# Kernel optimization log

Hardware: AMD Instinct MI355X
Metric: run time of the kernel (lower is better)

## Reference

```python
import jax, jax.numpy as jnp
import numpy as np

D = 768      # hidden size (hardcoded in module)
H = 8        # MHA heads
DH = D // H  # head dim = 96
SLOPE = 0.01 # LeakyReLU default negative slope
NEG = -1e9


def _leaky(x):
    return jnp.where(x >= 0, x, SLOPE * x)


def setup_inputs() -> dict:
    key = jax.random.key(0)
    ks = jax.random.split(key, 20)
    B, S, T, C, L = 32, 2048, 64, 512, 16
    seq = jax.random.normal(ks[0], (B, S, D), dtype=jnp.float32)
    tab_ids = jax.random.randint(ks[1], (B, T, L), 0, S, dtype=jnp.int32)
    col_ids = jax.random.randint(ks[2], (B, C, L), 0, S, dtype=jnp.int32)
    # contiguous column->table assignment (8 cols/table), mirrors cumulative
    # slicing by column_number_in_each_table and keeps every table non-empty
    t_of_c = jnp.broadcast_to(jnp.repeat(jnp.arange(T, dtype=jnp.int32), C // T), (B, C))
    g = lambda k, sh: (jax.random.normal(k, sh, dtype=jnp.float32) * 0.02)
    return {
        "sequence_embeddings": seq,
        "table_token_ids": tab_ids,
        "column_token_ids": col_ids,
        "table_of_column": t_of_c,
        "W_tab_pool": g(ks[3], (D, D)), "b_tab_pool": g(ks[4], (D,)),
        "W_col_pool": g(ks[5], (D, D)), "b_col_pool": g(ks[6], (D,)),
        "in_proj_w": g(ks[7], (3 * D, D)), "in_proj_b": g(ks[8], (3 * D,)),
        "out_proj_w": g(ks[9], (D, D)), "out_proj_b": g(ks[10], (D,)),
        "W_t1": g(ks[11], (D, 256)), "b_t1": g(ks[12], (256,)),
        "W_t2": g(ks[13], (256, 2)), "b_t2": g(ks[14], (2,)),
        "W_c1": g(ks[15], (D, 256)), "b_c1": g(ks[16], (256,)),
        "W_c2": g(ks[17], (256, 2)), "b_c2": g(ks[18], (2,)),
    }


def reference(sequence_embeddings, table_token_ids, column_token_ids, table_of_column,
              W_tab_pool, b_tab_pool, W_col_pool, b_col_pool,
              in_proj_w, in_proj_b, out_proj_w, out_proj_b,
              W_t1, b_t1, W_t2, b_t2, W_c1, b_c1, W_c2, b_c2):
    B, T = table_token_ids.shape[:2]
    C = column_token_ids.shape[1]
    bi = jnp.arange(B)[:, None, None]
    # ragged span sum-pooling (gather + segment sum)
    tab = sequence_embeddings[bi, table_token_ids].sum(axis=2)   # [B,T,D]
    col = sequence_embeddings[bi, column_token_ids].sum(axis=2)  # [B,C,D]
    tab = _leaky(tab @ W_tab_pool + b_tab_pool)
    col = _leaky(col @ W_col_pool + b_col_pool)
    # per-table cross-attention (table query over its own columns), batched + masked
    Wq, Wk, Wv = jnp.split(in_proj_w, 3, axis=0)
    bq, bk, bv = jnp.split(in_proj_b, 3, axis=0)
    q = (tab @ Wq.T + bq).reshape(B, T, H, DH)
    k = (col @ Wk.T + bk).reshape(B, C, H, DH)
    v = (col @ Wv.T + bv).reshape(B, C, H, DH)
    scores = jnp.einsum('bthd,bchd->bhtc', q, k) / jnp.sqrt(jnp.float32(DH))
    mask = table_of_column[:, None, None, :] == jnp.arange(T, dtype=table_of_column.dtype)[None, None, :, None]
    attn = jax.nn.softmax(jnp.where(mask, scores, NEG), axis=-1)
    ctx = jnp.einsum('bhtc,bchd->bthd', attn, v).reshape(B, T, D)
    tab = tab + (ctx @ out_proj_w.T + out_proj_b)
    tab = tab / jnp.maximum(jnp.linalg.norm(tab, axis=-1, keepdims=True), 1e-12)
    # classification heads (dropout in eval mode = identity)
    t_logits = _leaky(tab @ W_t1 + b_t1) @ W_t2 + b_t2  # [B,T,2]
    c_logits = _leaky(col @ W_c1 + b_c1) @ W_c2 + b_c2  # [B,C,2]
    return jnp.concatenate([t_logits, c_logits], axis=1)  # [B,T+C,2]
```

## Files before the change

### kernel.cpp

```cpp
#include <hip/hip_runtime.h>
#include <hip/hip_bf16.h>

constexpr int Bc = 32;
constexpr int Sc = 2048;
constexpr int Tc = 64;
constexpr int Cc = 512;
constexpr int Lc = 16;
constexpr int Dc = 768;
constexpr int Hc = 8;
constexpr int DHc = 96;

typedef __attribute__((ext_vector_type(4))) float f32x4;
typedef __attribute__((ext_vector_type(8))) short bf16x8;

__device__ inline unsigned short f2bf(float f) {
  __hip_bfloat16 h = __float2bfloat16(f);
  return *reinterpret_cast<unsigned short*>(&h);
}
__device__ inline float bf2f(__hip_bfloat16 h) { return __bfloat162float(h); }

#define GLDS16(gp, lp)                                                        \
  __builtin_amdgcn_global_load_lds(                                           \
      (const __attribute__((address_space(1))) void*)(gp),                    \
      (__attribute__((address_space(3))) void*)(lp), 16, 0, 0)

__global__ __launch_bounds__(256) void pool_kernel(
    const float* __restrict__ seq, const int* __restrict__ tab_ids,
    const int* __restrict__ col_ids, __hip_bfloat16* __restrict__ tabp,
    __hip_bfloat16* __restrict__ colp) {
  int w = threadIdx.x >> 6, l = threadIdx.x & 63;
  int row = blockIdx.x * 4 + w;
  int b = row / (Tc + Cc), r = row % (Tc + Cc);
  const int* ids;
  __hip_bfloat16* outp;
  if (r < Tc) {
    ids = tab_ids + ((size_t)b * Tc + r) * Lc;
    outp = tabp + ((size_t)b * Tc + r) * Dc;
  } else {
    int c = r - Tc;
    ids = col_ids + ((size_t)b * Cc + c) * Lc;
    outp = colp + ((size_t)b * Cc + c) * Dc;
  }
  float4 a0 = {0, 0, 0, 0}, a1 = {0, 0, 0, 0}, a2 = {0, 0, 0, 0};
#pragma unroll
  for (int t = 0; t < Lc; ++t) {
    const float4* p =
        reinterpret_cast<const float4*>(seq + ((size_t)b * Sc + ids[t]) * Dc);
    float4 v0 = p[l], v1 = p[l + 64], v2 = p[l + 128];
    a0.x += v0.x; a0.y += v0.y; a0.z += v0.z; a0.w += v0.w;
    a1.x += v1.x; a1.y += v1.y; a1.z += v1.z; a1.w += v1.w;
    a2.x += v2.x; a2.y += v2.y; a2.z += v2.z; a2.w += v2.w;
  }
  ushort4* ob = reinterpret_cast<ushort4*>(outp);
  ob[l] = make_ushort4(f2bf(a0.x), f2bf(a0.y), f2bf(a0.z), f2bf(a0.w));
  ob[l + 64] = make_ushort4(f2bf(a1.x), f2bf(a1.y), f2bf(a1.z), f2bf(a1.w));
  ob[l + 128] = make_ushort4(f2bf(a2.x), f2bf(a2.y), f2bf(a2.z), f2bf(a2.w));
}

__global__ __launch_bounds__(256) void convt_kernel(
    const float* __restrict__ in, __hip_bfloat16* __restrict__ out, int K,
    int N) {
  __shared__ float t[32][33];
  int bx = blockIdx.x * 32, by = blockIdx.y * 32;
  int x = threadIdx.x & 31, y = threadIdx.x >> 5;
#pragma unroll
  for (int i = 0; i < 32; i += 8) t[y + i][x] = in[(size_t)(by + y + i) * N + bx + x];
  __syncthreads();
#pragma unroll
  for (int i = 0; i < 32; i += 8)
    out[(size_t)(bx + y + i) * K + by + x] = __float2bfloat16(t[x][y + i]);
}

__global__ __launch_bounds__(256) void conv_kernel(
    const float4* __restrict__ in, ushort4* __restrict__ out, int n4) {
  int i = blockIdx.x * 256 + threadIdx.x;
  if (i < n4) {
    float4 v = in[i];
    out[i] = make_ushort4(f2bf(v.x), f2bf(v.y), f2bf(v.z), f2bf(v.w));
  }
}

template <int OUTMODE, bool LEAKY>
__global__ __launch_bounds__(256) void gemm_bf16(
    const __hip_bfloat16* __restrict__ A, const __hip_bfloat16* __restrict__ Bt,
    const float* __restrict__ bias, __hip_bfloat16* __restrict__ Obf,
    float* __restrict__ Of32, int M, int N, int K) {
  constexpr int BM = 128, BN = 128, BK = 32;
  __shared__ __hip_bfloat16 As[BM * BK];
  __shared__ __hip_bfloat16 Bs[BN * BK];
  int tid = threadIdx.x;
  int row0 = blockIdx.y * BM, col0 = blockIdx.x * BN;
  int w = tid >> 6, l = tid & 63;
  int wr = (w >> 1) * 64, wc = (w & 1) * 64;
  f32x4 acc[4][4];
#pragma unroll
  for (int m = 0; m < 4; ++m)
#pragma unroll
    for (int n = 0; n < 4; ++n) acc[m][n] = f32x4{0.f, 0.f, 0.f, 0.f};

  int srow = tid >> 2;
  int skk = (tid & 3) * 8;
  const __hip_bfloat16* gA = A + (size_t)(row0 + srow) * K + skk;
  const __hip_bfloat16* gB = Bt + (size_t)(col0 + srow) * K + skk;
  char* lA = (char*)As + tid * 16;
  char* lB = (char*)Bs + tid * 16;
  int lr = l & 15, lk = (l >> 4) * 8;

  for (int k0 = 0; k0 < K; k0 += BK) {
    GLDS16(gA + k0, lA);
    GLDS16(gA + k0 + (size_t)64 * K, lA + 4096);
    GLDS16(gB + k0, lB);
    GLDS16(gB + k0 + (size_t)64 * K, lB + 4096);
    __syncthreads();
    bf16x8 af[4], bfr[4];
#pragma unroll
    for (int m = 0; m < 4; ++m)
      af[m] = *reinterpret_cast<const bf16x8*>(&As[(wr + m * 16 + lr) * BK + lk]);
#pragma unroll
    for (int n = 0; n < 4; ++n)
      bfr[n] = *reinterpret_cast<const bf16x8*>(&Bs[(wc + n * 16 + lr) * BK + lk]);
#pragma unroll
    for (int m = 0; m < 4; ++m)
#pragma unroll
      for (int n = 0; n < 4; ++n)
        acc[m][n] = __builtin_amdgcn_mfma_f32_16x16x32_bf16(af[m], bfr[n],
                                                            acc[m][n], 0, 0, 0);
    __syncthreads();
  }

  int colI = l & 15, rowb = (l >> 4) * 4;
#pragma unroll
  for (int m = 0; m < 4; ++m) {
#pragma unroll
    for (int n = 0; n < 4; ++n) {
      int c = col0 + wc + n * 16 + colI;
      float bv = bias ? bias[c] : 0.f;
#pragma unroll
      for (int j = 0; j < 4; ++j) {
        int r = row0 + wr + m * 16 + rowb + j;
        float v = acc[m][n][j] + bv;
        if (LEAKY) v = v >= 0.f ? v : 0.01f * v;
        if (OUTMODE == 0 || OUTMODE == 2)
          Obf[(size_t)r * N + c] = __float2bfloat16(v);
        if (OUTMODE == 1 || OUTMODE == 2) Of32[(size_t)r * N + c] = v;
      }
    }
  }
}

__global__ __launch_bounds__(256) void bucket_kernel(
    const int* __restrict__ t_of_c, int* __restrict__ col_sorted,
    int* __restrict__ offs) {
  int b = blockIdx.x, tid = threadIdx.x;
  __shared__ int cnt[Tc];
  __shared__ int cur[Tc + 1];
  if (tid < Tc) cnt[tid] = 0;
  __syncthreads();
  for (int c = tid; c < Cc; c += 256) atomicAdd(&cnt[t_of_c[b * Cc + c]], 1);
  __syncthreads();
  if (tid == 0) {
    int off = 0;
    for (int t = 0; t < Tc; ++t) {
      cur[t] = off;
      off += cnt[t];
    }
    cur[Tc] = off;
  }
  __syncthreads();
  if (tid <= Tc) offs[b * (Tc + 1) + tid] = cur[tid];
  __syncthreads();
  for (int c = tid; c < Cc; c += 256) {
    int t = t_of_c[b * Cc + c];
    int pos = atomicAdd(&cur[t], 1);
    col_sorted[b * Cc + pos] = c;
  }
}

__global__ __launch_bounds__(256) void attn_kernel(
    const __hip_bfloat16* __restrict__ q, const __hip_bfloat16* __restrict__ kv,
    const int* __restrict__ col_sorted, const int* __restrict__ offs,
    __hip_bfloat16* __restrict__ ctx) {
  int b = blockIdx.x / Tc;
  int t = blockIdx.x % Tc;
  __shared__ float qs[Dc];
  __shared__ float pbuf[Hc][Cc];
  __shared__ float den[Hc];
  __shared__ int cols_s[Cc];
  int tid = threadIdx.x;
  for (int i = tid; i < Dc; i += 256)
    qs[i] = bf2f(q[((size_t)b * Tc + t) * Dc + i]);
  int o0 = offs[b * (Tc + 1) + t];
  int o1 = offs[b * (Tc + 1) + t + 1];
  int n = o1 - o0;
  for (int i = tid; i < n; i += 256)
    cols_s[i] = col_sorted[(size_t)b * Cc + o0 + i];
  __syncthreads();
  int h = tid >> 5, l32 = tid & 31;
  const float scale = 0.10206207261596577f;
  if (n > 0) {
    float lmax = -3.0e38f;
    for (int j = l32; j < n; j += 32) {
      const __hip_bfloat16* kr = kv + ((size_t)b * Cc + cols_s[j]) * 1536 + h * DHc;
      float s = 0.f;
#pragma unroll 8
      for (int d = 0; d < DHc; ++d) s += qs[h * DHc + d] * bf2f(kr[d]);
      s *= scale;
      pbuf[h][j] = s;
      lmax = fmaxf(lmax, s);
    }
#pragma unroll
    for (int m = 16; m >= 1; m >>= 1) lmax = fmaxf(lmax, __shfl_xor(lmax, m));
    float lsum = 0.f;
    for (int j = l32; j < n; j += 32) {
      float e = __expf(pbuf[h][j] - lmax);
      pbuf[h][j] = e;
      lsum += e;
    }
#pragma unroll
    for (int m = 16; m >= 1; m >>= 1) lsum += __shfl_xor(lsum, m);
    if (l32 == 0) den[h] = lsum;
  }
  __syncthreads();
#pragma unroll
  for (int rep = 0; rep < 3; ++rep) {
    int d = l32 + rep * 32;
    float acc = 0.f;
    if (n > 0) {
      for (int j = 0; j < n; ++j)
        acc += pbuf[h][j] *
               bf2f(kv[((size_t)b * Cc + cols_s[j]) * 1536 + 768 + h * DHc + d]);
      acc /= den[h];
    } else {
      for (int c = 0; c < Cc; ++c)
        acc += bf2f(kv[((size_t)b * Cc + c) * 1536 + 768 + h * DHc + d]);
      acc *= (1.0f / Cc);
    }
    ctx[((size_t)b * Tc + t) * Dc + h * DHc + d] = __float2bfloat16(acc);
  }
}

__global__ __launch_bounds__(256) void addnorm_kernel(
    const float* __restrict__ tab, const float* __restrict__ proj,
    __hip_bfloat16* __restrict__ tabn) {
  int row = blockIdx.x;
  int tid = threadIdx.x;
  size_t base = (size_t)row * Dc;
  float x0 = tab[base + tid] + proj[base + tid];
  float x1 = tab[base + tid + 256] + proj[base + tid + 256];
  float x2 = tab[base + tid + 512] + proj[base + tid + 512];
  float ss = x0 * x0 + x1 * x1 + x2 * x2;
#pragma unroll
  for (int m = 32; m >= 1; m >>= 1) ss += __shfl_xor(ss, m);
  __shared__ float red[4];
  int wave = tid >> 6, lane = tid & 63;
  if (lane == 0) red[wave] = ss;
  __syncthreads();
  float total = red[0] + red[1] + red[2] + red[3];
  float sc = 1.0f / fmaxf(sqrtf(total), 1e-12f);
  tabn[base + tid] = __float2bfloat16(x0 * sc);
  tabn[base + tid + 256] = __float2bfloat16(x1 * sc);
  tabn[base + tid + 512] = __float2bfloat16(x2 * sc);
}

__global__ __launch_bounds__(256) void head2_kernel(
    const float* __restrict__ h1t, const float* __restrict__ h1c,
    const float* __restrict__ W_t2, const float* __restrict__ b_t2,
    const float* __restrict__ W_c2, const float* __restrict__ b_c2,
    float* __restrict__ out) {
  int w = threadIdx.x >> 6;
  int lane = threadIdx.x & 63;
  int row = blockIdx.x * 4 + w;
  int b = row / (Tc + Cc);
  int r = row % (Tc + Cc);
  const float* h1;
  const float* W2;
  const float* b2;
  if (r < Tc) {
    h1 = h1t + ((size_t)b * Tc + r) * 256;
    W2 = W_t2;
    b2 = b_t2;
  } else {
    h1 = h1c + ((size_t)b * Cc + (r - Tc)) * 256;
    W2 = W_c2;
    b2 = b_c2;
  }
  float a0 = 0.f, a1 = 0.f;
  for (int i = lane; i < 256; i += 64) {
    float x = h1[i];
    a0 += x * W2[2 * i];
    a1 += x * W2[2 * i + 1];
  }
#pragma unroll
  for (int m = 32; m >= 1; m >>= 1) {
    a0 += __shfl_xor(a0, m);
    a1 += __shfl_xor(a1, m);
  }
  if (lane == 0) {
    out[(size_t)row * 2] = a0 + b2[0];
    out[(size_t)row * 2 + 1] = a1 + b2[1];
  }
}

extern "C" void kernel_launch(void* const* d_in, const int* in_sizes, int n_in,
                              void* d_out, int out_size, void* d_ws,
                              size_t ws_size, hipStream_t stream) {
  const float* seq = (const float*)d_in[0];
  const int* tab_ids = (const int*)d_in[1];
  const int* col_ids = (const int*)d_in[2];
  const int* t_of_c = (const int*)d_in[3];
  const float* W_tab_pool = (const float*)d_in[4];
  const float* b_tab_pool = (const float*)d_in[5];
  const float* W_col_pool = (const float*)d_in[6];
  const float* b_col_pool = (const float*)d_in[7];
  const float* in_proj_w = (const float*)d_in[8];
  const float* in_proj_b = (const float*)d_in[9];
  const float* out_proj_w = (const float*)d_in[10];
  const float* out_proj_b = (const float*)d_in[11];
  const float* W_t1 = (const float*)d_in[12];
  const float* b_t1 = (const float*)d_in[13];
  const float* W_t2 = (const float*)d_in[14];
  const float* b_t2 = (const float*)d_in[15];
  const float* W_c1 = (const float*)d_in[16];
  const float* b_c1 = (const float*)d_in[17];
  const float* W_c2 = (const float*)d_in[18];
  const float* b_c2 = (const float*)d_in[19];
  float* out = (float*)d_out;

  typedef __hip_bfloat16 bf;
  char* p = (char*)d_ws;
  auto alloc = [&](size_t bytes) -> char* {
    char* r = p;
    p += (bytes + 255) & ~(size_t)255;
    return r;
  };
  const size_t nBT = (size_t)Bc * Tc;
  const size_t nBC = (size_t)Bc * Cc;
  bf* tabp = (bf*)alloc(nBT * Dc * 2);
  bf* colp = (bf*)alloc(nBC * Dc * 2);
  bf* tabb_bf = (bf*)alloc(nBT * Dc * 2);
  float* tabb_f = (float*)alloc(nBT * Dc * 4);
  bf* colb = (bf*)alloc(nBC * Dc * 2);
  bf* qb = (bf*)alloc(nBT * Dc * 2);
  bf* kvb = (bf*)alloc(nBC * 1536 * 2);
  bf* ctxb = (bf*)alloc(nBT * Dc * 2);
  float* projb = (float*)alloc(nBT * Dc * 4);
  bf* tabn = (bf*)alloc(nBT * Dc * 2);
  float* h1t = (float*)alloc(nBT * 256 * 4);
  float* h1c = (float*)alloc(nBC * 256 * 4);
  bf* wtab_t = (bf*)alloc((size_t)Dc * Dc * 2);
  bf* wcol_t = (bf*)alloc((size_t)Dc * Dc * 2);
  bf* winproj = (bf*)alloc((size_t)3 * Dc * Dc * 2);
  bf* woutproj = (bf*)alloc((size_t)Dc * Dc * 2);
  bf* wt1_t = (bf*)alloc((size_t)256 * Dc * 2);
  bf* wc1_t = (bf*)alloc((size_t)256 * Dc * 2);
  int* col_sorted = (int*)alloc(nBC * 4);
  int* offs = (int*)alloc((size_t)Bc * (Tc + 1) * 4);

  convt_kernel<<<dim3(Dc / 32, Dc / 32), 256, 0, stream>>>(W_tab_pool, wtab_t, Dc, Dc);
  convt_kernel<<<dim3(Dc / 32, Dc / 32), 256, 0, stream>>>(W_col_pool, wcol_t, Dc, Dc);
  conv_kernel<<<(3 * Dc * Dc / 4) / 256, 256, 0, stream>>>(
      (const float4*)in_proj_w, (ushort4*)winproj, 3 * Dc * Dc / 4);
  conv_kernel<<<(Dc * Dc / 4) / 256, 256, 0, stream>>>(
      (const float4*)out_proj_w, (ushort4*)woutproj, Dc * Dc / 4);
  convt_kernel<<<dim3(256 / 32, Dc / 32), 256, 0, stream>>>(W_t1, wt1_t, Dc, 256);
  convt_kernel<<<dim3(256 / 32, Dc / 32), 256, 0, stream>>>(W_c1, wc1_t, Dc, 256);

  bucket_kernel<<<Bc, 256, 0, stream>>>(t_of_c, col_sorted, offs);
  pool_kernel<<<Bc * (Tc + Cc) / 4, 256, 0, stream>>>(seq, tab_ids, col_ids,
                                                      tabp, colp);
  gemm_bf16<2, true><<<dim3(Dc / 128, nBT / 128), 256, 0, stream>>>(
      tabp, wtab_t, b_tab_pool, tabb_bf, tabb_f, nBT, Dc, Dc);
  gemm_bf16<0, true><<<dim3(Dc / 128, nBC / 128), 256, 0, stream>>>(
      colp, wcol_t, b_col_pool, colb, nullptr, nBC, Dc, Dc);
  gemm_bf16<0, false><<<dim3(Dc / 128, nBT / 128), 256, 0, stream>>>(
      tabb_bf, winproj, in_proj_b, qb, nullptr, nBT, Dc, Dc);
  gemm_bf16<0, false><<<dim3(1536 / 128, nBC / 128), 256, 0, stream>>>(
      colb, winproj + (size_t)Dc * Dc, in_proj_b + Dc, kvb, nullptr, nBC, 1536,
      Dc);
  attn_kernel<<<Bc * Tc, 256, 0, stream>>>(qb, kvb, col_sorted, offs, ctxb);
  gemm_bf16<1, false><<<dim3(Dc / 128, nBT / 128), 256, 0, stream>>>(
      ctxb, woutproj, out_proj_b, nullptr, projb, nBT, Dc, Dc);
  addnorm_kernel<<<nBT, 256, 0, stream>>>(tabb_f, projb, tabn);
  gemm_bf16<1, true><<<dim3(256 / 128, nBT / 128), 256, 0, stream>>>(
      tabn, wt1_t, b_t1, nullptr, h1t, nBT, 256, Dc);
  gemm_bf16<1, true><<<dim3(256 / 128, nBC / 128), 256, 0, stream>>>(
      colb, wc1_t, b_c1, nullptr, h1c, nBC, 256, Dc);
  head2_kernel<<<(Bc * (Tc + Cc)) / 4, 256, 0, stream>>>(h1t, h1c, W_t2, b_t2,
                                                         W_c2, b_c2, out);
}
```

Measured before the change: 627.4 us.

## Fuse weight prep, fold head2 into GEMM epilogue, rework attention and GEMM BK

Merges the six weight-conversion launches and the output bias initialisation into one prep kernel. Fuses the second classifier layer into the first head GEMM's epilogue, which reduces across lanes and atomically adds into the output, so the h1 buffers and the head2 kernel go away. Rewrites attention so 8-lane groups use vectorised bf16 loads with q held in registers for both QK and PV, and doubles the GEMM K-tile to 64. It also swizzles the pool kernel's block order. Atomics make the output summation order nondeterministic, and the larger tile raises LDS use.

```diff
diff --git a/kernel.cpp b/kernel.cpp
--- a/kernel.cpp
+++ b/kernel.cpp
@@ -12,27 +12,82 @@
 
 typedef __attribute__((ext_vector_type(4))) float f32x4;
 typedef __attribute__((ext_vector_type(8))) short bf16x8;
+typedef __hip_bfloat16 bf;
 
 __device__ inline unsigned short f2bf(float f) {
   __hip_bfloat16 h = __float2bfloat16(f);
   return *reinterpret_cast<unsigned short*>(&h);
 }
-__device__ inline float bf2f(__hip_bfloat16 h) { return __bfloat162float(h); }
+__device__ inline float us2f(unsigned short u) {
+  return __uint_as_float(((unsigned)u) << 16);
+}
 
 #define GLDS16(gp, lp)                                                        \
   __builtin_amdgcn_global_load_lds(                                           \
       (const __attribute__((address_space(1))) void*)(gp),                    \
       (__attribute__((address_space(3))) void*)(lp), 16, 0, 0)
 
+__device__ inline void transpose32(const float* __restrict__ in,
+                                   bf* __restrict__ outp, int K, int N,
+                                   int ti, float (*t)[33]) {
+  int nx = N >> 5;
+  int bx = (ti % nx) * 32, by = (ti / nx) * 32;
+  int x = threadIdx.x & 31, y = threadIdx.x >> 5;
+#pragma unroll
+  for (int i = 0; i < 32; i += 8)
+    t[y + i][x] = in[(size_t)(by + y + i) * N + bx + x];
+  __syncthreads();
+#pragma unroll
+  for (int i = 0; i < 32; i += 8)
+    outp[(size_t)(bx + y + i) * K + by + x] = __float2bfloat16(t[x][y + i]);
+}
+
+__global__ __launch_bounds__(256) void prep_kernel(
+    const float* __restrict__ W_tab_pool, const float* __restrict__ W_col_pool,
+    const float* __restrict__ W_t1, const float* __restrict__ W_c1,
+    const float* __restrict__ in_proj_w, const float* __restrict__ out_proj_w,
+    const float* __restrict__ b_t2, const float* __restrict__ b_c2,
+    bf* __restrict__ wtab_t, bf* __restrict__ wcol_t, bf* __restrict__ wt1_t,
+    bf* __restrict__ wc1_t, bf* __restrict__ winproj, bf* __restrict__ woutproj,
+    float* __restrict__ outd) {
+  __shared__ float t[32][33];
+  int blk = blockIdx.x, tid = threadIdx.x;
+  if (blk < 576) {
+    transpose32(W_tab_pool, wtab_t, Dc, Dc, blk, t);
+  } else if (blk < 1152) {
+    transpose32(W_col_pool, wcol_t, Dc, Dc, blk - 576, t);
+  } else if (blk < 1344) {
+    transpose32(W_t1, wt1_t, Dc, 256, blk - 1152, t);
+  } else if (blk < 1536) {
+    transpose32(W_c1, wc1_t, Dc, 256, blk - 1344, t);
+  } else if (blk < 3264) {
+    int i = (blk - 1536) * 256 + tid;
+    float4 v = reinterpret_cast<const float4*>(in_proj_w)[i];
+    reinterpret_cast<ushort4*>(winproj)[i] =
+        make_ushort4(f2bf(v.x), f2bf(v.y), f2bf(v.z), f2bf(v.w));
+  } else if (blk < 3840) {
+    int i = (blk - 3264) * 256 + tid;
+    float4 v = reinterpret_cast<const float4*>(out_proj_w)[i];
+    reinterpret_cast<ushort4*>(woutproj)[i] =
+        make_ushort4(f2bf(v.x), f2bf(v.y), f2bf(v.z), f2bf(v.w));
+  } else {
+    int e = (blk - 3840) * 256 + tid;
+    int i = e & 1;
+    int r = (e >> 1) % (Tc + Cc);
+    outd[e] = (r < Tc) ? b_t2[i] : b_c2[i];
+  }
+}
+
 __global__ __launch_bounds__(256) void pool_kernel(
     const float* __restrict__ seq, const int* __restrict__ tab_ids,
-    const int* __restrict__ col_ids, __hip_bfloat16* __restrict__ tabp,
-    __hip_bfloat16* __restrict__ colp) {
+    const int* __restrict__ col_ids, bf* __restrict__ tabp,
+    bf* __restrict__ colp) {
+  int swz = (blockIdx.x & 7) * 576 + (blockIdx.x >> 3);
   int w = threadIdx.x >> 6, l = threadIdx.x & 63;
-  int row = blockIdx.x * 4 + w;
+  int row = swz * 4 + w;
   int b = row / (Tc + Cc), r = row % (Tc + Cc);
   const int* ids;
-  __hip_bfloat16* outp;
+  bf* outp;
   if (r < Tc) {
     ids = tab_ids + ((size_t)b * Tc + r) * Lc;
     outp = tabp + ((size_t)b * Tc + r) * Dc;
@@ -43,9 +98,9 @@
   }
   float4 a0 = {0, 0, 0, 0}, a1 = {0, 0, 0, 0}, a2 = {0, 0, 0, 0};
 #pragma unroll
-  for (int t = 0; t < Lc; ++t) {
+  for (int tix = 0; tix < Lc; ++tix) {
     const float4* p =
-        reinterpret_cast<const float4*>(seq + ((size_t)b * Sc + ids[t]) * Dc);
+        reinterpret_cast<const float4*>(seq + ((size_t)b * Sc + ids[tix]) * Dc);
     float4 v0 = p[l], v1 = p[l + 64], v2 = p[l + 128];
     a0.x += v0.x; a0.y += v0.y; a0.z += v0.z; a0.w += v0.w;
     a1.x += v1.x; a1.y += v1.y; a1.z += v1.z; a1.w += v1.w;
@@ -57,37 +112,15 @@
   ob[l + 128] = make_ushort4(f2bf(a2.x), f2bf(a2.y), f2bf(a2.z), f2bf(a2.w));
 }
 
-__global__ __launch_bounds__(256) void convt_kernel(
-    const float* __restrict__ in, __hip_bfloat16* __restrict__ out, int K,
-    int N) {
-  __shared__ float t[32][33];
-  int bx = blockIdx.x * 32, by = blockIdx.y * 32;
-  int x = threadIdx.x & 31, y = threadIdx.x >> 5;
-#pragma unroll
-  for (int i = 0; i < 32; i += 8) t[y + i][x] = in[(size_t)(by + y + i) * N + bx + x];
-  __syncthreads();
-#pragma unroll
-  for (int i = 0; i < 32; i += 8)
-    out[(size_t)(bx + y + i) * K + by + x] = __float2bfloat16(t[x][y + i]);
-}
-
-__global__ __launch_bounds__(256) void conv_kernel(
-    const float4* __restrict__ in, ushort4* __restrict__ out, int n4) {
-  int i = blockIdx.x * 256 + threadIdx.x;
-  if (i < n4) {
-    float4 v = in[i];
-    out[i] = make_ushort4(f2bf(v.x), f2bf(v.y), f2bf(v.z), f2bf(v.w));
-  }
-}
-
-template <int OUTMODE, bool LEAKY>
+template <int OUTMODE, bool LEAKY, int LOG2RPB>
 __global__ __launch_bounds__(256) void gemm_bf16(
-    const __hip_bfloat16* __restrict__ A, const __hip_bfloat16* __restrict__ Bt,
-    const float* __restrict__ bias, __hip_bfloat16* __restrict__ Obf,
-    float* __restrict__ Of32, int M, int N, int K) {
-  constexpr int BM = 128, BN = 128, BK = 32;
-  __shared__ __hip_bfloat16 As[BM * BK];
-  __shared__ __hip_bfloat16 Bs[BN * BK];
+    const bf* __restrict__ A, const bf* __restrict__ Bt,
+    const float* __restrict__ bias, bf* __restrict__ Obf,
+    float* __restrict__ Of32, const float* __restrict__ w2,
+    float* __restrict__ outd, int out_base, int M, int N, int K) {
+  constexpr int BM = 128, BN = 128, BK = 64;
+  __shared__ bf As[BM * BK];
+  __shared__ bf Bs[BN * BK];
   int tid = threadIdx.x;
   int row0 = blockIdx.y * BM, col0 = blockIdx.x * BN;
   int w = tid >> 6, l = tid & 63;
@@ -98,37 +131,94 @@
 #pragma unroll
     for (int n = 0; n < 4; ++n) acc[m][n] = f32x4{0.f, 0.f, 0.f, 0.f};
 
-  int srow = tid >> 2;
-  int skk = (tid & 3) * 8;
-  const __hip_bfloat16* gA = A + (size_t)(row0 + srow) * K + skk;
-  const __hip_bfloat16* gB = Bt + (size_t)(col0 + srow) * K + skk;
+  int srow = tid >> 3, skk = (tid & 7) * 8;
+  const bf* gA = A + (size_t)(row0 + srow) * K + skk;
+  const bf* gB = Bt + (size_t)(col0 + srow) * K + skk;
   char* lA = (char*)As + tid * 16;
   char* lB = (char*)Bs + tid * 16;
   int lr = l & 15, lk = (l >> 4) * 8;
 
   for (int k0 = 0; k0 < K; k0 += BK) {
-    GLDS16(gA + k0, lA);
-    GLDS16(gA + k0 + (size_t)64 * K, lA + 4096);
-    GLDS16(gB + k0, lB);
-    GLDS16(gB + k0 + (size_t)64 * K, lB + 4096);
+#pragma unroll
+    for (int c = 0; c < 4; ++c) {
+      GLDS16(gA + k0 + (size_t)c * 32 * K, lA + c * 4096);
+      GLDS16(gB + k0 + (size_t)c * 32 * K, lB + c * 4096);
+    }
     __syncthreads();
-    bf16x8 af[4], bfr[4];
+    bf16x8 af[2][4], bfr[2][4];
+#pragma unroll
+    for (int ks = 0; ks < 2; ++ks) {
+#pragma unroll
+      for (int m = 0; m < 4; ++m)
+        af[ks][m] = *reinterpret_cast<const bf16x8*>(
+            &As[(wr + m * 16 + lr) * BK + ks * 32 + lk]);
+#pragma unroll
+      for (int n = 0; n < 4; ++n)
+        bfr[ks][n] = *reinterpret_cast<const bf16x8*>(
+            &Bs[(wc + n * 16 + lr) * BK + ks * 32 + lk]);
+    }
+#pragma unroll
+    for (int ks = 0; ks < 2; ++ks)
+#pragma unroll
+      for (int m = 0; m < 4; ++m)
+#pragma unroll
+        for (int n = 0; n < 4; ++n)
+          acc[m][n] = __builtin_amdgcn_mfma_f32_16x16x32_bf16(
+              af[ks][m], bfr[ks][n], acc[m][n], 0, 0, 0);
+    __syncthreads();
+  }
+
+  int colI = l & 15, rowb = (l >> 4) * 4;
+  if (OUTMODE == 3) {
+    float w20[4], w21[4], bv[4];
+#pragma unroll
+    for (int n = 0; n < 4; ++n) {
+      int c = col0 + wc + n * 16 + colI;
+      w20[n] = w2[c * 2];
+      w21[n] = w2[c * 2 + 1];
+      bv[n] = bias[c];
+    }
+    float p0[4][4], p1[4][4];
 #pragma unroll
     for (int m = 0; m < 4; ++m)
-      af[m] = *reinterpret_cast<const bf16x8*>(&As[(wr + m * 16 + lr) * BK + lk]);
-#pragma unroll
-    for (int n = 0; n < 4; ++n)
-      bfr[n] = *reinterpret_cast<const bf16x8*>(&Bs[(wc + n * 16 + lr) * BK + lk]);
+#pragma unroll
+      for (int j = 0; j < 4; ++j) { p0[m][j] = 0.f; p1[m][j] = 0.f; }
 #pragma unroll
     for (int m = 0; m < 4; ++m)
 #pragma unroll
       for (int n = 0; n < 4; ++n)
-        acc[m][n] = __builtin_amdgcn_mfma_f32_16x16x32_bf16(af[m], bfr[n],
-                                                            acc[m][n], 0, 0, 0);
-    __syncthreads();
-  }
-
-  int colI = l & 15, rowb = (l >> 4) * 4;
+#pragma unroll
+        for (int j = 0; j < 4; ++j) {
+          float v = acc[m][n][j] + bv[n];
+          v = v >= 0.f ? v : 0.01f * v;
+          p0[m][j] += v * w20[n];
+          p1[m][j] += v * w21[n];
+        }
+#pragma unroll
+    for (int m = 0; m < 4; ++m)
+#pragma unroll
+      for (int j = 0; j < 4; ++j) {
+#pragma unroll
+        for (int msk = 1; msk <= 8; msk <<= 1) {
+          p0[m][j] += __shfl_xor(p0[m][j], msk);
+          p1[m][j] += __shfl_xor(p1[m][j], msk);
+        }
+      }
+    if (colI == 0) {
+#pragma unroll
+      for (int m = 0; m < 4; ++m)
+#pragma unroll
+        for (int j = 0; j < 4; ++j) {
+          int grow = row0 + wr + m * 16 + rowb + j;
+          int bb = grow >> LOG2RPB;
+          int rr = grow & ((1 << LOG2RPB) - 1);
+          int orow = bb * (Tc + Cc) + out_base + rr;
+          atomicAdd(&outd[(size_t)orow * 2], p0[m][j]);
+          atomicAdd(&outd[(size_t)orow * 2 + 1], p1[m][j]);
+        }
+    }
+    return;
+  }
 #pragma unroll
   for (int m = 0; m < 4; ++m) {
 #pragma unroll
@@ -177,37 +267,59 @@
 }
 
 __global__ __launch_bounds__(256) void attn_kernel(
-    const __hip_bfloat16* __restrict__ q, const __hip_bfloat16* __restrict__ kv,
+    const bf* __restrict__ q, const bf* __restrict__ kv,
     const int* __restrict__ col_sorted, const int* __restrict__ offs,
-    __hip_bfloat16* __restrict__ ctx) {
+    bf* __restrict__ ctx) {
   int b = blockIdx.x / Tc;
   int t = blockIdx.x % Tc;
-  __shared__ float qs[Dc];
   __shared__ float pbuf[Hc][Cc];
   __shared__ float den[Hc];
   __shared__ int cols_s[Cc];
   int tid = threadIdx.x;
-  for (int i = tid; i < Dc; i += 256)
-    qs[i] = bf2f(q[((size_t)b * Tc + t) * Dc + i]);
   int o0 = offs[b * (Tc + 1) + t];
-  int o1 = offs[b * (Tc + 1) + t + 1];
-  int n = o1 - o0;
+  int n = offs[b * (Tc + 1) + t + 1] - o0;
   for (int i = tid; i < n; i += 256)
     cols_s[i] = col_sorted[(size_t)b * Cc + o0 + i];
   __syncthreads();
-  int h = tid >> 5, l32 = tid & 31;
+  int h = tid >> 5, l32 = tid & 31, g = l32 >> 3, i8 = l32 & 7;
   const float scale = 0.10206207261596577f;
+  float q12[12];
+  {
+    const ushort* qp = (const ushort*)q + ((size_t)b * Tc + t) * Dc + h * DHc + i8 * 12;
+    ushort4 u0 = *(const ushort4*)(qp);
+    ushort4 u1 = *(const ushort4*)(qp + 4);
+    ushort4 u2 = *(const ushort4*)(qp + 8);
+    q12[0] = us2f(u0.x); q12[1] = us2f(u0.y); q12[2] = us2f(u0.z); q12[3] = us2f(u0.w);
+    q12[4] = us2f(u1.x); q12[5] = us2f(u1.y); q12[6] = us2f(u1.z); q12[7] = us2f(u1.w);
+    q12[8] = us2f(u2.x); q12[9] = us2f(u2.y); q12[10] = us2f(u2.z); q12[11] = us2f(u2.w);
+  }
+  if (n > 0) {
+    for (int jb = 0; jb < n; jb += 4) {
+      int j = jb + g;
+      float s = 0.f;
+      if (j < n) {
+        const ushort* kp =
+            (const ushort*)kv + ((size_t)b * Cc + cols_s[j]) * 1536 + h * DHc + i8 * 12;
+        ushort4 u0 = *(const ushort4*)(kp);
+        ushort4 u1 = *(const ushort4*)(kp + 4);
+        ushort4 u2 = *(const ushort4*)(kp + 8);
+        s += q12[0] * us2f(u0.x) + q12[1] * us2f(u0.y) + q12[2] * us2f(u0.z) +
+             q12[3] * us2f(u0.w);
+        s += q12[4] * us2f(u1.x) + q12[5] * us2f(u1.y) + q12[6] * us2f(u1.z) +
+             q12[7] * us2f(u1.w);
+        s += q12[8] * us2f(u2.x) + q12[9] * us2f(u2.y) + q12[10] * us2f(u2.z) +
+             q12[11] * us2f(u2.w);
+      }
+      s += __shfl_xor(s, 1);
+      s += __shfl_xor(s, 2);
+      s += __shfl_xor(s, 4);
+      if (j < n && i8 == 0) pbuf[h][j] = s * scale;
+    }
+  }
+  __syncthreads();
   if (n > 0) {
     float lmax = -3.0e38f;
-    for (int j = l32; j < n; j += 32) {
-      const __hip_bfloat16* kr = kv + ((size_t)b * Cc + cols_s[j]) * 1536 + h * DHc;
-      float s = 0.f;
-#pragma unroll 8
-      for (int d = 0; d < DHc; ++d) s += qs[h * DHc + d] * bf2f(kr[d]);
-      s *= scale;
-      pbuf[h][j] = s;
-      lmax = fmaxf(lmax, s);
-    }
+    for (int j = l32; j < n; j += 32) lmax = fmaxf(lmax, pbuf[h][j]);
 #pragma unroll
     for (int m = 16; m >= 1; m >>= 1) lmax = fmaxf(lmax, __shfl_xor(lmax, m));
     float lsum = 0.f;
@@ -219,29 +331,55 @@
 #pragma unroll
     for (int m = 16; m >= 1; m >>= 1) lsum += __shfl_xor(lsum, m);
     if (l32 == 0) den[h] = lsum;
-  }
-  __syncthreads();
-#pragma unroll
-  for (int rep = 0; rep < 3; ++rep) {
-    int d = l32 + rep * 32;
-    float acc = 0.f;
-    if (n > 0) {
-      for (int j = 0; j < n; ++j)
-        acc += pbuf[h][j] *
-               bf2f(kv[((size_t)b * Cc + cols_s[j]) * 1536 + 768 + h * DHc + d]);
-      acc /= den[h];
-    } else {
-      for (int c = 0; c < Cc; ++c)
-        acc += bf2f(kv[((size_t)b * Cc + c) * 1536 + 768 + h * DHc + d]);
-      acc *= (1.0f / Cc);
-    }
-    ctx[((size_t)b * Tc + t) * Dc + h * DHc + d] = __float2bfloat16(acc);
+  } else if (l32 == 0) {
+    den[h] = (float)Cc;
+  }
+  __syncthreads();
+  int ncols = n > 0 ? n : Cc;
+  float a12[12];
+#pragma unroll
+  for (int d = 0; d < 12; ++d) a12[d] = 0.f;
+  for (int jb = 0; jb < ncols; jb += 4) {
+    int j = jb + g;
+    if (j < ncols) {
+      int cj = n > 0 ? cols_s[j] : j;
+      float pw = n > 0 ? pbuf[h][j] : 1.f;
+      const ushort* vp =
+          (const ushort*)kv + ((size_t)b * Cc + cj) * 1536 + 768 + h * DHc + i8 * 12;
+      ushort4 u0 = *(const ushort4*)(vp);
+      ushort4 u1 = *(const ushort4*)(vp + 4);
+      ushort4 u2 = *(const ushort4*)(vp + 8);
+      a12[0] += pw * us2f(u0.x); a12[1] += pw * us2f(u0.y);
+      a12[2] += pw * us2f(u0.z); a12[3] += pw * us2f(u0.w);
+      a12[4] += pw * us2f(u1.x); a12[5] += pw * us2f(u1.y);
+      a12[6] += pw * us2f(u1.z); a12[7] += pw * us2f(u1.w);
+      a12[8] += pw * us2f(u2.x); a12[9] += pw * us2f(u2.y);
+      a12[10] += pw * us2f(u2.z); a12[11] += pw * us2f(u2.w);
+    }
+  }
+#pragma unroll
+  for (int d = 0; d < 12; ++d) {
+    a12[d] += __shfl_xor(a12[d], 8);
+    a12[d] += __shfl_xor(a12[d], 16);
+  }
+  float inv = 1.0f / den[h];
+  if (g == 0) {
+    ushort* cp = (ushort*)ctx + ((size_t)b * Tc + t) * Dc + h * DHc + i8 * 12;
+    ushort4 o0 = make_ushort4(f2bf(a12[0] * inv), f2bf(a12[1] * inv),
+                              f2bf(a12[2] * inv), f2bf(a12[3] * inv));
+    ushort4 o1 = make_ushort4(f2bf(a12[4] * inv), f2bf(a12[5] * inv),
+                              f2bf(a12[6] * inv), f2bf(a12[7] * inv));
+    ushort4 o2 = make_ushort4(f2bf(a12[8] * inv), f2bf(a12[9] * inv),
+                              f2bf(a12[10] * inv), f2bf(a12[11] * inv));
+    *(ushort4*)(cp) = o0;
+    *(ushort4*)(cp + 4) = o1;
+    *(ushort4*)(cp + 8) = o2;
   }
 }
 
 __global__ __launch_bounds__(256) void addnorm_kernel(
     const float* __restrict__ tab, const float* __restrict__ proj,
-    __hip_bfloat16* __restrict__ tabn) {
+    bf* __restrict__ tabn) {
   int row = blockIdx.x;
   int tid = threadIdx.x;
   size_t base = (size_t)row * Dc;
@@ -260,45 +398,6 @@
   tabn[base + tid] = __float2bfloat16(x0 * sc);
   tabn[base + tid + 256] = __float2bfloat16(x1 * sc);
   tabn[base + tid + 512] = __float2bfloat16(x2 * sc);
-}
-
-__global__ __launch_bounds__(256) void head2_kernel(
-    const float* __restrict__ h1t, const float* __restrict__ h1c,
-    const float* __restrict__ W_t2, const float* __restrict__ b_t2,
-    const float* __restrict__ W_c2, const float* __restrict__ b_c2,
-    float* __restrict__ out) {
-  int w = threadIdx.x >> 6;
-  int lane = threadIdx.x & 63;
-  int row = blockIdx.x * 4 + w;
-  int b = row / (Tc + Cc);
-  int r = row % (Tc + Cc);
-  const float* h1;
-  const float* W2;
-  const float* b2;
-  if (r < Tc) {
-    h1 = h1t + ((size_t)b * Tc + r) * 256;
-    W2 = W_t2;
-    b2 = b_t2;
-  } else {
-    h1 = h1c + ((size_t)b * Cc + (r - Tc)) * 256;
-    W2 = W_c2;
-    b2 = b_c2;
-  }
-  float a0 = 0.f, a1 = 0.f;
-  for (int i = lane; i < 256; i += 64) {
-    float x = h1[i];
-    a0 += x * W2[2 * i];
-    a1 += x * W2[2 * i + 1];
-  }
-#pragma unroll
-  for (int m = 32; m >= 1; m >>= 1) {
-    a0 += __shfl_xor(a0, m);
-    a1 += __shfl_xor(a1, m);
-  }
-  if (lane == 0) {
-    out[(size_t)row * 2] = a0 + b2[0];
-    out[(size_t)row * 2 + 1] = a1 + b2[1];
-  }
 }
 
 extern "C" void kernel_launch(void* const* d_in, const int* in_sizes, int n_in,
@@ -326,7 +425,6 @@
   const float* b_c2 = (const float*)d_in[19];
   float* out = (float*)d_out;
 
-  typedef __hip_bfloat16 bf;
   char* p = (char*)d_ws;
   auto alloc = [&](size_t bytes) -> char* {
     char* r = p;
@@ -345,8 +443,6 @@
   bf* ctxb = (bf*)alloc(nBT * Dc * 2);
   float* projb = (float*)alloc(nBT * Dc * 4);
   bf* tabn = (bf*)alloc(nBT * Dc * 2);
-  float* h1t = (float*)alloc(nBT * 256 * 4);
-  float* h1c = (float*)alloc(nBC * 256 * 4);
   bf* wtab_t = (bf*)alloc((size_t)Dc * Dc * 2);
   bf* wcol_t = (bf*)alloc((size_t)Dc * Dc * 2);
   bf* winproj = (bf*)alloc((size_t)3 * Dc * Dc * 2);
@@ -356,35 +452,32 @@
   int* col_sorted = (int*)alloc(nBC * 4);
   int* offs = (int*)alloc((size_t)Bc * (Tc + 1) * 4);
 
-  convt_kernel<<<dim3(Dc / 32, Dc / 32), 256, 0, stream>>>(W_tab_pool, wtab_t, Dc, Dc);
-  convt_kernel<<<dim3(Dc / 32, Dc / 32), 256, 0, stream>>>(W_col_pool, wcol_t, Dc, Dc);
-  conv_kernel<<<(3 * Dc * Dc / 4) / 256, 256, 0, stream>>>(
-      (const float4*)in_proj_w, (ushort4*)winproj, 3 * Dc * Dc / 4);
-  conv_kernel<<<(Dc * Dc / 4) / 256, 256, 0, stream>>>(
-      (const float4*)out_proj_w, (ushort4*)woutproj, Dc * Dc / 4);
-  convt_kernel<<<dim3(256 / 32, Dc / 32), 256, 0, stream>>>(W_t1, wt1_t, Dc, 256);
-  convt_kernel<<<dim3(256 / 32, Dc / 32), 256, 0, stream>>>(W_c1, wc1_t, Dc, 256);
-
+  prep_kernel<<<3984, 256, 0, stream>>>(W_tab_pool, W_col_pool, W_t1, W_c1,
+                                        in_proj_w, out_proj_w, b_t2, b_c2,
+                                        wtab_t, wcol_t, wt1_t, wc1_t, winproj,
+                                        woutproj, out);
   bucket_kernel<<<Bc, 256, 0, stream>>>(t_of_c, col_sorted, offs);
   pool_kernel<<<Bc * (Tc + Cc) / 4, 256, 0, stream>>>(seq, tab_ids, col_ids,
                                                       tabp, colp);
-  gemm_bf16<2, true><<<dim3(Dc / 128, nBT / 128), 256, 0, stream>>>(
-      tabp, wtab_t, b_tab_pool, tabb_bf, tabb_f, nBT, Dc, Dc);
-  gemm_bf16<0, true><<<dim3(Dc / 128, nBC / 128), 256, 0, stream>>>(
-      colp, wcol_t, b_col_pool, colb, nullptr, nBC, Dc, Dc);
-  gemm_bf16<0, false><<<dim3(Dc / 128, nBT / 128), 256, 0, stream>>>(
-      tabb_bf, winproj, in_proj_b, qb, nullptr, nBT, Dc, Dc);
-  gemm_bf16<0, false><<<dim3(1536 / 128, nBC / 128), 256, 0, stream>>>(
-      colb, winproj + (size_t)Dc * Dc, in_proj_b + Dc, kvb, nullptr, nBC, 1536,
+  gemm_bf16<2, true, 0><<<dim3(Dc / 128, nBT / 128), 256, 0, stream>>>(
+      tabp, wtab_t, b_tab_pool, tabb_bf, tabb_f, nullptr, nullptr, 0, nBT, Dc,
       Dc);
+  gemm_bf16<0, true, 0><<<dim3(Dc / 128, nBC / 128), 256, 0, stream>>>(
+      colp, wcol_t, b_col_pool, colb, nullptr, nullptr, nullptr, 0, nBC, Dc,
+      Dc);
+  gemm_bf16<0, false, 0><<<dim3(Dc / 128, nBT / 128), 256, 0, stream>>>(
+      tabb_bf, winproj, in_proj_b, qb, nullptr, nullptr, nullptr, 0, nBT, Dc,
+      Dc);
+  gemm_bf16<0, false, 0><<<dim3(1536 / 128, nBC / 128), 256, 0, stream>>>(
+      colb, winproj + (size_t)Dc * Dc, in_proj_b + Dc, kvb, nullptr, nullptr,
+      nullptr, 0, nBC, 1536, Dc);
   attn_kernel<<<Bc * Tc, 256, 0, stream>>>(qb, kvb, col_sorted, offs, ctxb);
-  gemm_bf16<1, false><<<dim3(Dc / 128, nBT / 128), 256, 0, stream>>>(
-      ctxb, woutproj, out_proj_b, nullptr, projb, nBT, Dc, Dc);
+  gemm_bf16<1, false, 0><<<dim3(Dc / 128, nBT / 128), 256, 0, stream>>>(
+      ctxb, woutproj, out_proj_b, nullptr, projb, nullptr, nullptr, 0, nBT, Dc,
+      Dc);
   addnorm_kernel<<<nBT, 256, 0, stream>>>(tabb_f, projb, tabn);
-  gemm_bf16<1, true><<<dim3(256 / 128, nBT / 128), 256, 0, stream>>>(
-      tabn, wt1_t, b_t1, nullptr, h1t, nBT, 256, Dc);
-  gemm_bf16<1, true><<<dim3(256 / 128, nBC / 128), 256, 0, stream>>>(
-      colb, wc1_t, b_c1, nullptr, h1c, nBC, 256, Dc);
-  head2_kernel<<<(Bc * (Tc + Cc)) / 4, 256, 0, stream>>>(h1t, h1c, W_t2, b_t2,
-                                                         W_c2, b_c2, out);
-}
+  gemm_bf16<3, true, 6><<<dim3(256 / 128, nBT / 128), 256, 0, stream>>>(
+      tabn, wt1_t, b_t1, nullptr, nullptr, W_t2, out, 0, nBT, 256, Dc);
+  gemm_bf16<3, true, 9><<<dim3(256 / 128, nBC / 128), 256, 0, stream>>>(
+      colb, wc1_t, b_c1, nullptr, nullptr, W_c2, out, Tc, nBC, 256, Dc);
+}
```

After: 603.6 us. 3.8% less time.
